# Kernel tuning notes

Measured on AMD Instinct MI355X. Metric: run time of the kernel, lower is better.

The kernel has to match this reference:

```python
import jax, jax.numpy as jnp
import numpy as np

N = 50000
E = 800000
P = 16
H = 128
NUM_LAYERS = 2


def _lin_params(key, fan_in, fan_out):
    k1, k2 = jax.random.split(key)
    bound = 1.0 / np.sqrt(fan_in)
    W = jax.random.uniform(k1, (fan_in, fan_out), jnp.float32, -bound, bound)
    b = jax.random.uniform(k2, (fan_out,), jnp.float32, -bound, bound)
    return W, b


def setup_inputs() -> dict:
    key = jax.random.key(0)
    ks = jax.random.split(key, 16)
    h = jax.random.normal(ks[0], (N, P), jnp.float32)
    x = jax.random.normal(ks[1], (N, 2), jnp.float32)
    edge_index = jax.random.randint(ks[2], (2, E), 0, N, jnp.int32)
    emb_W, emb_b = _lin_params(ks[3], P, H)
    e_W1, e_b1 = _lin_params(ks[4], 2 * H + 1, H)
    e_W2, e_b2 = _lin_params(ks[5], H, H)
    n_W1, n_b1 = _lin_params(ks[6], 2 * H, H)
    n_W2, n_b2 = _lin_params(ks[7], H, H)
    v_W1, v_b1 = _lin_params(ks[8], H, H)
    v_W2, v_b2 = _lin_params(ks[9], H, 2)
    c_W1, c_b1 = _lin_params(ks[10], H, H)
    c_W2, c_b2 = _lin_params(ks[11], H, 1)
    return dict(h=h, x=x, edge_index=edge_index,
                emb_W=emb_W, emb_b=emb_b,
                e_W1=e_W1, e_b1=e_b1, e_W2=e_W2, e_b2=e_b2,
                n_W1=n_W1, n_b1=n_b1, n_W2=n_W2, n_b2=n_b2,
                v_W1=v_W1, v_b1=v_b1, v_W2=v_W2, v_b2=v_b2,
                c_W1=c_W1, c_b1=c_b1, c_W2=c_W2, c_b2=c_b2)


def _mlp(z, W1, b1, W2, b2):
    return jnp.maximum(z @ W1 + b1, 0.0) @ W2 + b2


def reference(h, x, edge_index, emb_W, emb_b,
              e_W1, e_b1, e_W2, e_b2,
              n_W1, n_b1, n_W2, n_b2,
              v_W1, v_b1, v_W2, v_b2,
              c_W1, c_b1, c_W2, c_b2):
    row, col = edge_index[0], edge_index[1]
    n_nodes = h.shape[0]
    # edge count per source node for scatter-mean (0-count nodes stay 0)
    cnt = jax.ops.segment_sum(jnp.ones((row.shape[0],), h.dtype), row,
                              num_segments=n_nodes)
    denom = jnp.maximum(cnt, 1.0)[:, None]

    h = h @ emb_W + emb_b  # [N, H]
    v = None
    for _ in range(NUM_LAYERS):
        rel_pos = x[row] - x[col]                         # [E, 2]
        rel_dist = jnp.sum(rel_pos ** 2, axis=-1, keepdims=True)  # [E, 1]
        rel_theta = jnp.arctan2(rel_pos[:, 1], rel_pos[:, 0])     # [E]
        rel_pos2 = rel_dist * jnp.stack(
            [jnp.cos(2.0 * rel_theta), jnp.sin(2.0 * rel_theta)], axis=1)  # [E, 2]
        edge_feat = jnp.concatenate([h[row], h[col], rel_dist], axis=-1)   # [E, 2H+1]
        m_ij = _mlp(edge_feat, e_W1, e_b1, e_W2, e_b2)    # [E, H] (dropout = eval identity)
        m_i = jax.ops.segment_sum(m_ij, row, num_segments=n_nodes)  # [N, H]
        h = h + _mlp(jnp.concatenate([h, m_i], axis=-1), n_W1, n_b1, n_W2, n_b2)
        v = _mlp(h, v_W1, v_b1, v_W2, v_b2)               # [N, 2]
        coord = _mlp(m_ij, c_W1, c_b1, c_W2, c_b2)        # [E, 1]
        scat = jax.ops.segment_sum(rel_pos2 * coord, row, num_segments=n_nodes)
        v = v + scat / denom                              # scatter-mean
    # F.normalize(p=2, dim=-1, eps=1e-12)
    norm = jnp.linalg.norm(v, axis=-1, keepdims=True)
    v = v / jnp.maximum(norm, 1e-12)
    return h, x, v
```

## Files before the change

### kernel.cpp

```cpp
#include <hip/hip_runtime.h>
#include <hip/hip_fp16.h>

typedef _Float16 f16;
typedef unsigned short u16;
typedef f16 f16x2 __attribute__((ext_vector_type(2)));
typedef f16 f16x8 __attribute__((ext_vector_type(8)));
typedef float f32x4 __attribute__((ext_vector_type(4)));

constexpr int N_NODES = 50000;
constexpr int E_EDGES = 800000;
constexpr int NBINS   = 50176;
constexpr int NBLK    = 196;

constexpr size_t OFF_DEG   = 0;
constexpr size_t OFF_LOCEX = 200704;
constexpr size_t OFF_BSUM  = 401408;
constexpr size_t OFF_BOFF  = 402432;
constexpr size_t OFF_FILL  = 403456;
constexpr size_t OFF_SCAT  = 604160;
constexpr size_t OFF_SROW  = 1004160;
constexpr size_t OFF_SCOL  = 2604160;
constexpr size_t OFF_ZSUM  = 4204160;
constexpr size_t ZSH_BYTES = (size_t)N_NODES * 128 * 2;
constexpr size_t ZS_BYTES  = (size_t)N_NODES * 128 * 4;
constexpr size_t OFF_APRE  = OFF_ZSUM + ZS_BYTES;
constexpr size_t OFF_BPRE  = OFF_APRE + (size_t)N_NODES * 128 * 2;
constexpr size_t OFF_CMB   = OFF_BPRE + (size_t)N_NODES * 128 * 2;
constexpr size_t OFF_WX    = OFF_CMB + 65536;
constexpr size_t OFF_BVEC  = OFF_WX + 65536;
constexpr size_t OFF_BX    = OFF_BVEC + 512;
constexpr size_t OFF_WSWZ  = OFF_BX + 512;

__device__ __forceinline__ void split_f(float x, f16& h, f16& l) {
    h = (f16)x;
    l = (f16)(x - (float)h);
}

__device__ __forceinline__ f32x4 mfma3(f16x8 ah, f16x8 al, f16x8 bh, f16x8 bl, f32x4 acc) {
    acc = __builtin_amdgcn_mfma_f32_16x16x32_f16(ah, bh, acc, 0, 0, 0);
    acc = __builtin_amdgcn_mfma_f32_16x16x32_f16(al, bh, acc, 0, 0, 0);
    acc = __builtin_amdgcn_mfma_f32_16x16x32_f16(ah, bl, acc, 0, 0, 0);
    return acc;
}

__device__ __forceinline__ void pk_atomic_add(f16* addr, float a0, float a1) {
    __half2 hv = __floats2half2_rn(a0, a1);
    unsafeAtomicAdd((__half2*)addr, hv);
}

__global__ __launch_bounds__(256) void compose_kernel(
    const float* __restrict__ eW2, const float* __restrict__ eb2,
    const float* __restrict__ nW1, const float* __restrict__ cW1,
    const float* __restrict__ cb1,
    float* __restrict__ Wcmb, float* __restrict__ Wx,
    float* __restrict__ bvec, float* __restrict__ bx)
{
    const int gid = blockIdx.x * 256 + threadIdx.x;
    if (gid < 16384) {
        const int k = gid >> 7, j = gid & 127;
        float s = 0.f;
        for (int t2 = 0; t2 < 128; ++t2) s += eW2[k * 128 + t2] * nW1[(128 + t2) * 128 + j];
        Wcmb[gid] = s;
    } else if (gid < 32768) {
        const int e = gid - 16384;
        const int k = e >> 7, j = e & 127;
        float s = 0.f;
        for (int t2 = 0; t2 < 128; ++t2) s += eW2[k * 128 + t2] * cW1[t2 * 128 + j];
        Wx[e] = s;
    } else if (gid < 32896) {
        const int j = gid - 32768;
        float s = 0.f;
        for (int k = 0; k < 128; ++k) s += eb2[k] * nW1[(128 + k) * 128 + j];
        bvec[j] = s;
    } else if (gid < 33024) {
        const int j = gid - 32896;
        float s = cb1[j];
        for (int k = 0; k < 128; ++k) s += eb2[k] * cW1[k * 128 + j];
        bx[j] = s;
    }
}

__global__ __launch_bounds__(256) void prep_kernel(
    const float* __restrict__ eW1, const float* __restrict__ nW1,
    const float* __restrict__ nW2, const float* __restrict__ vW1,
    const float* __restrict__ Wcmb, const float* __restrict__ Wx,
    f16* __restrict__ Wpres, f16* __restrict__ nW1cs,
    f16* __restrict__ nW2s, f16* __restrict__ vW1s, f16* __restrict__ Wxs)
{
    const int gid = blockIdx.x * 256 + threadIdx.x;
    int K32, e, which; f16* out;
    if (gid < 32768)       { which = 0; out = Wpres; K32 = 4; e = gid; }
    else if (gid < 65536)  { which = 1; out = nW1cs; K32 = 8; e = gid - 32768; }
    else if (gid < 81920)  { which = 2; out = nW2s;  K32 = 4; e = gid - 65536; }
    else if (gid < 98304)  { which = 3; out = vW1s;  K32 = 4; e = gid - 81920; }
    else                   { which = 4; out = Wxs;   K32 = 4; e = gid - 98304; }
    const int per = 512 * K32;
    const int ct = e / per, rem = e % per;
    const int kk = rem >> 9, lane = (rem >> 3) & 63, j = rem & 7;
    const int col = ct * 16 + (lane & 15);
    const int k = kk * 32 + ((lane >> 4) & 3) * 8 + j;
    float v;
    if (which == 0)      v = (col < 128) ? eW1[k * 128 + col] : eW1[(128 + k) * 128 + (col - 128)];
    else if (which == 1) v = (k < 128) ? nW1[k * 128 + col] : Wcmb[(k - 128) * 128 + col];
    else if (which == 2) v = nW2[k * 128 + col];
    else if (which == 3) v = vW1[k * 128 + col];
    else                 v = Wx[k * 128 + col];
    f16 h, l; split_f(v, h, l);
    const int base = ((ct * K32 + kk) * 2) * 512 + lane * 8 + j;
    out[base] = h;
    out[base + 512] = l;
}

__global__ __launch_bounds__(256) void hist_kernel(const int* __restrict__ eidx,
                                                   int* __restrict__ deg) {
    const int e = blockIdx.x * 256 + threadIdx.x;
    if (e < E_EDGES) atomicAdd(&deg[eidx[e]], 1);
}

__global__ __launch_bounds__(256) void scan1_kernel(const int* __restrict__ deg,
                                                    int* __restrict__ locEx,
                                                    int* __restrict__ blockSum) {
    __shared__ int s[256];
    const int t = threadIdx.x;
    const int gid = blockIdx.x * 256 + t;
    const int v = deg[gid];
    s[t] = v;
    __syncthreads();
    for (int off = 1; off < 256; off <<= 1) {
        const int add = (t >= off) ? s[t - off] : 0;
        __syncthreads();
        s[t] += add;
        __syncthreads();
    }
    locEx[gid] = s[t] - v;
    if (t == 255) blockSum[blockIdx.x] = s[255];
}

__global__ __launch_bounds__(256) void scan2_kernel(const int* __restrict__ blockSum,
                                                    int* __restrict__ blockOff) {
    __shared__ int s[256];
    const int t = threadIdx.x;
    const int v = (t < NBLK) ? blockSum[t] : 0;
    s[t] = v;
    __syncthreads();
    for (int off = 1; off < 256; off <<= 1) {
        const int add = (t >= off) ? s[t - off] : 0;
        __syncthreads();
        s[t] += add;
        __syncthreads();
    }
    if (t < NBLK) blockOff[t] = s[t] - v;
}

__global__ __launch_bounds__(256) void scatter_kernel(const int* __restrict__ eidx,
        const int* __restrict__ locEx, const int* __restrict__ blockOff,
        int* __restrict__ fill, u16* __restrict__ srow, u16* __restrict__ scol) {
    const int e = blockIdx.x * 256 + threadIdx.x;
    if (e >= E_EDGES) return;
    const int r = eidx[e], c = eidx[E_EDGES + e];
    const int pos = blockOff[r >> 8] + locEx[r] + atomicAdd(&fill[r], 1);
    srow[pos] = (u16)r;
    scol[pos] = (u16)c;
}

__global__ __launch_bounds__(256) void embed_kernel(
    const float* __restrict__ h_in, const float* __restrict__ embW,
    const float* __restrict__ embb, float* __restrict__ h)
{
    const int gid = blockIdx.x * 256 + threadIdx.x;
    if (gid >= N_NODES * 128) return;
    const int n = gid >> 7, j = gid & 127;
    float s = embb[j];
#pragma unroll
    for (int p = 0; p < 16; ++p) s += h_in[n * 16 + p] * embW[p * 128 + j];
    h[gid] = s;
}

__device__ __forceinline__ void stage8(const float* src, f16* dst) {
    const float4 f0 = *(const float4*)src;
    const float4 f1 = *(const float4*)(src + 4);
    const float xs[8] = {f0.x, f0.y, f0.z, f0.w, f1.x, f1.y, f1.z, f1.w};
    f16x8 vh, vl;
#pragma unroll
    for (int i = 0; i < 8; ++i) { f16 hh, ll; split_f(xs[i], hh, ll); vh[i] = hh; vl[i] = ll; }
    *(f16x8*)dst = vh;
    *(f16x8*)(dst + 8) = vl;
}

__global__ __launch_bounds__(256, 4) void pre_kernel(
    const float* __restrict__ h, const f16* __restrict__ Wpres,
    const float* __restrict__ eb1,
    f16* __restrict__ Apre, f16* __restrict__ Bpre)
{
    constexpr int S = 264;
    __shared__ f16 smA[64 * S];
    const int t = threadIdx.x;
    const int base = blockIdx.x * 64;
    const int lane = t & 63, w = t >> 6, qq = lane >> 4, nn = lane & 15;

#pragma unroll
    for (int it = 0; it < 4; ++it) {
        const int idx = it * 256 + t;
        const int el = idx >> 4, seg = idx & 15;
        const int node = base + el;
        f16* dst = &smA[el * S + seg * 16];
        if (node < N_NODES) {
            stage8(h + (size_t)node * 128 + seg * 8, dst);
        } else {
            *(f16x8*)dst = (f16x8)(f16)0.f;
            *(f16x8*)(dst + 8) = (f16x8)(f16)0.f;
        }
    }
    __syncthreads();

#pragma unroll
    for (int half = 0; half < 2; ++half) {
        f32x4 acc[4][2] = {};
        for (int kk = 0; kk < 4; ++kk) {
            f16x8 Ah[4], Al[4];
#pragma unroll
            for (int rt = 0; rt < 4; ++rt) {
                const f16* ap = &smA[(rt * 16 + nn) * S + (kk * 4 + qq) * 16];
                Ah[rt] = *(const f16x8*)ap;
                Al[rt] = *(const f16x8*)(ap + 8);
            }
#pragma unroll
            for (int c = 0; c < 2; ++c) {
                const int ct = w * 4 + half * 2 + c;
                const f16* bp = Wpres + (size_t)((ct * 4 + kk) * 2) * 512 + lane * 8;
                const f16x8 Bh = *(const f16x8*)bp;
                const f16x8 Bl = *(const f16x8*)(bp + 512);
#pragma unroll
                for (int rt = 0; rt < 4; ++rt)
                    acc[rt][c] = mfma3(Ah[rt], Al[rt], Bh, Bl, acc[rt][c]);
            }
        }
#pragma unroll
        for (int c = 0; c < 2; ++c) {
            const int col = w * 64 + half * 32 + c * 16 + nn;
#pragma unroll
            for (int rt = 0; rt < 4; ++rt) {
#pragma unroll
                for (int r = 0; r < 4; ++r) {
                    const int el = rt * 16 + qq * 4 + r;
                    const int node = base + el;
                    if (node < N_NODES) {
                        const float v = acc[rt][c][r];
                        if (col < 128) Apre[(size_t)node * 128 + col] = (f16)(v + eb1[col]);
                        else           Bpre[(size_t)node * 128 + (col - 128)] = (f16)v;
                    }
                }
            }
        }
    }
}

__global__ __launch_bounds__(256, 8) void edge_z_kernel(
    const u16* __restrict__ srow, const u16* __restrict__ scol,
    const float* __restrict__ x,
    const f16* __restrict__ Apre, const f16* __restrict__ Bpre,
    const float* __restrict__ wlast,
    f16* __restrict__ zsumh)
{
    constexpr int S2 = 136;
    __shared__ f16 smZ[64 * S2];
    __shared__ int smRow[64], smCol[64];
    __shared__ float smRd[64];
    const int t = threadIdx.x;
    const int base = blockIdx.x * 64;
    if (t < 64) {
        const int e = base + t;
        const int r = (int)srow[e], c = (int)scol[e];
        smRow[t] = r; smCol[t] = c;
        const float dx = x[2 * r] - x[2 * c];
        const float dy = x[2 * r + 1] - x[2 * c + 1];
        smRd[t] = dx * dx + dy * dy;
    }
    __syncthreads();

    const int seg = t & 15;
    const float4 w0 = *(const float4*)(wlast + seg * 8);
    const float4 w1 = *(const float4*)(wlast + seg * 8 + 4);
    const float wl[8] = {w0.x, w0.y, w0.z, w0.w, w1.x, w1.y, w1.z, w1.w};
#pragma unroll
    for (int it = 0; it < 4; ++it) {
        const int el = it * 16 + (t >> 4);
        const int rn = smRow[el], cn = smCol[el];
        const f16x8 av = *(const f16x8*)(Apre + (size_t)rn * 128 + seg * 8);
        const f16x8 bv = *(const f16x8*)(Bpre + (size_t)cn * 128 + seg * 8);
        const float rd = smRd[el];
        f16x8 vz;
#pragma unroll
        for (int i = 0; i < 8; ++i)
            vz[i] = (f16)fmaxf((float)av[i] + (float)bv[i] + rd * wl[i], 0.f);
        *(f16x8*)&smZ[el * S2 + seg * 8] = vz;
    }
    __syncthreads();

    const int p = t & 63, g = t >> 6;
    float a0 = 0.f, a1 = 0.f;
    int prev = smRow[g * 16];
#pragma unroll
    for (int e = g * 16; e < g * 16 + 16; ++e) {
        const int rw = smRow[e];
        if (rw != prev) {
            pk_atomic_add(&zsumh[(size_t)prev * 128 + 2 * p], a0, a1);
            a0 = a1 = 0.f; prev = rw;
        }
        const f16x2 v = *(const f16x2*)&smZ[e * S2 + 2 * p];
        a0 += (float)v[0]; a1 += (float)v[1];
    }
    pk_atomic_add(&zsumh[(size_t)prev * 128 + 2 * p], a0, a1);
}

__global__ __launch_bounds__(256, 8) void edge_coord_kernel(
    const u16* __restrict__ srow, const u16* __restrict__ scol,
    const float* __restrict__ x,
    const f16* __restrict__ Apre, const f16* __restrict__ Bpre,
    const float* __restrict__ wlast,
    const f16* __restrict__ Wxs, const float* __restrict__ bx,
    const float* __restrict__ cW2, const float* __restrict__ cb2,
    f16* __restrict__ zsumh, float* __restrict__ scat)
{
    constexpr int S2 = 136;
    __shared__ f16 smZ[64 * S2];
    __shared__ int smRow[64], smCol[64];
    __shared__ float smRd[64], smP2x[64], smP2y[64];
    __shared__ float smPart[4][64];

    const int t = threadIdx.x;
    const int base = blockIdx.x * 64;
    const int lane = t & 63, w = t >> 6, qq = lane >> 4, nn = lane & 15;

    if (t < 64) {
        const int e = base + t;
        const int r = (int)srow[e], c = (int)scol[e];
        smRow[t] = r; smCol[t] = c;
        const float dx = x[2 * r] - x[2 * c];
        const float dy = x[2 * r + 1] - x[2 * c + 1];
        smRd[t] = dx * dx + dy * dy;
        smP2x[t] = dx * dx - dy * dy;
        smP2y[t] = 2.0f * dx * dy;
    }
    __syncthreads();

    {
        const int seg = t & 15;
        const float4 w0 = *(const float4*)(wlast + seg * 8);
        const float4 w1 = *(const float4*)(wlast + seg * 8 + 4);
        const float wl[8] = {w0.x, w0.y, w0.z, w0.w, w1.x, w1.y, w1.z, w1.w};
#pragma unroll
        for (int it = 0; it < 4; ++it) {
            const int el = it * 16 + (t >> 4);
            const int rn = smRow[el], cn = smCol[el];
            const f16x8 av = *(const f16x8*)(Apre + (size_t)rn * 128 + seg * 8);
            const f16x8 bv = *(const f16x8*)(Bpre + (size_t)cn * 128 + seg * 8);
            const float rd = smRd[el];
            f16x8 vz;
#pragma unroll
            for (int i = 0; i < 8; ++i)
                vz[i] = (f16)fmaxf((float)av[i] + (float)bv[i] + rd * wl[i], 0.f);
            *(f16x8*)&smZ[el * S2 + seg * 8] = vz;
        }
    }
    __syncthreads();

    {
        const int p = t & 63, g = t >> 6;
        float a0 = 0.f, a1 = 0.f;
        int prev = smRow[g * 16];
#pragma unroll
        for (int e = g * 16; e < g * 16 + 16; ++e) {
            const int rw = smRow[e];
            if (rw != prev) {
                pk_atomic_add(&zsumh[(size_t)prev * 128 + 2 * p], a0, a1);
                a0 = a1 = 0.f; prev = rw;
            }
            const f16x2 v = *(const f16x2*)&smZ[e * S2 + 2 * p];
            a0 += (float)v[0]; a1 += (float)v[1];
        }
        pk_atomic_add(&zsumh[(size_t)prev * 128 + 2 * p], a0, a1);
    }

    f32x4 acc3[4][2] = {};
    for (int kk = 0; kk < 4; ++kk) {
        f16x8 A[4];
#pragma unroll
        for (int rt = 0; rt < 4; ++rt)
            A[rt] = *(const f16x8*)&smZ[(rt * 16 + nn) * S2 + (kk * 4 + qq) * 8];
#pragma unroll
        for (int c = 0; c < 2; ++c) {
            const int ct = w * 2 + c;
            const f16x8 Bh = *(const f16x8*)(Wxs + (size_t)((ct * 4 + kk) * 2) * 512 + lane * 8);
#pragma unroll
            for (int rt = 0; rt < 4; ++rt)
                acc3[rt][c] = __builtin_amdgcn_mfma_f32_16x16x32_f16(A[rt], Bh, acc3[rt][c], 0, 0, 0);
        }
    }
    float p3[4][4];
#pragma unroll
    for (int rt = 0; rt < 4; ++rt)
#pragma unroll
        for (int r = 0; r < 4; ++r) p3[rt][r] = 0.f;
#pragma unroll
    for (int c = 0; c < 2; ++c) {
        const int col = w * 32 + c * 16 + nn;
        const float c1 = bx[col];
        const float w2 = cW2[col];
#pragma unroll
        for (int rt = 0; rt < 4; ++rt)
#pragma unroll
            for (int r = 0; r < 4; ++r)
                p3[rt][r] += fmaxf(acc3[rt][c][r] + c1, 0.f) * w2;
    }
#pragma unroll
    for (int off = 1; off < 16; off <<= 1)
#pragma unroll
        for (int rt = 0; rt < 4; ++rt)
#pragma unroll
            for (int r = 0; r < 4; ++r) p3[rt][r] += __shfl_xor(p3[rt][r], off);
    if (nn == 0) {
#pragma unroll
        for (int rt = 0; rt < 4; ++rt)
#pragma unroll
            for (int r = 0; r < 4; ++r)
                smPart[w][rt * 16 + qq * 4 + r] = p3[rt][r];
    }
    __syncthreads();
    if (t < 64) {
        const float co = smPart[0][t] + smPart[1][t] + smPart[2][t] + smPart[3][t] + cb2[0];
        const int rw = smRow[t];
        atomicAdd(&scat[2 * rw],     smP2x[t] * co);
        atomicAdd(&scat[2 * rw + 1], smP2y[t] * co);
    }
}

__global__ __launch_bounds__(256, 4) void node_kernel(
    float* __restrict__ h, f16* __restrict__ zsumh,
    const int* __restrict__ deg,
    const f16* __restrict__ nW1cs, const float* __restrict__ nb1,
    const float* __restrict__ bvec,
    const f16* __restrict__ nW2s, const float* __restrict__ nb2)
{
    constexpr int S = 264;
    __shared__ f16 smA[64 * S];
    __shared__ float smDeg[64];
    const int t = threadIdx.x;
    const int base = blockIdx.x * 64;
    const int lane = t & 63, w = t >> 6, qq = lane >> 4, nn = lane & 15;

    if (t < 64) smDeg[t] = (float)deg[base + t];

    f32x4 acc1[4][2] = {};
    for (int chunk = 0; chunk < 2; ++chunk) {
        if (chunk) __syncthreads();
#pragma unroll
        for (int it = 0; it < 4; ++it) {
            const int idx = it * 256 + t;
            const int el = idx >> 4, seg = idx & 15;
            const int node = base + el;
            f16* dst = &smA[el * S + seg * 16];
            if (node < N_NODES) {
                if (chunk == 0) {
                    stage8(h + (size_t)node * 128 + seg * 8, dst);
                } else {
                    f16* src = zsumh + (size_t)node * 128 + seg * 8;
                    const f16x8 v = *(const f16x8*)src;
                    *(f16x8*)dst = v;
                    *(f16x8*)(dst + 8) = (f16x8)(f16)0.f;
                    *(f16x8*)src = (f16x8)(f16)0.f;
                }
            } else {
                *(f16x8*)dst = (f16x8)(f16)0.f;
                *(f16x8*)(dst + 8) = (f16x8)(f16)0.f;
            }
        }
        __syncthreads();
        for (int kk = 0; kk < 4; ++kk) {
            f16x8 Ah[4], Al[4];
#pragma unroll
            for (int rt = 0; rt < 4; ++rt) {
                const f16* ap = &smA[(rt * 16 + nn) * S + (kk * 4 + qq) * 16];
                Ah[rt] = *(const f16x8*)ap;
                Al[rt] = *(const f16x8*)(ap + 8);
            }
            const int kkg = chunk * 4 + kk;
#pragma unroll
            for (int c = 0; c < 2; ++c) {
                const int ct = w * 2 + c;
                const f16* bp = nW1cs + (size_t)((ct * 8 + kkg) * 2) * 512 + lane * 8;
                const f16x8 Bh = *(const f16x8*)bp;
                const f16x8 Bl = *(const f16x8*)(bp + 512);
#pragma unroll
                for (int rt = 0; rt < 4; ++rt)
                    acc1[rt][c] = mfma3(Ah[rt], Al[rt], Bh, Bl, acc1[rt][c]);
            }
        }
    }
    __syncthreads();
#pragma unroll
    for (int c = 0; c < 2; ++c) {
        const int col = w * 32 + c * 16 + nn;
        const float b1 = nb1[col];
        const float bv = bvec[col];
#pragma unroll
        for (int rt = 0; rt < 4; ++rt) {
#pragma unroll
            for (int r = 0; r < 4; ++r) {
                const int el = rt * 16 + qq * 4 + r;
                const float z = fmaxf(acc1[rt][c][r] + b1 + smDeg[el] * bv, 0.f);
                f16 zh, zl; split_f(z, zh, zl);
                f16* zp = &smA[el * S + (col >> 3) * 16 + (col & 7)];
                zp[0] = zh; zp[8] = zl;
            }
        }
    }
    __syncthreads();

    f32x4 acc2[4][2] = {};
    for (int kk = 0; kk < 4; ++kk) {
        f16x8 Ah[4], Al[4];
#pragma unroll
        for (int rt = 0; rt < 4; ++rt) {
            const f16* ap = &smA[(rt * 16 + nn) * S + (kk * 4 + qq) * 16];
            Ah[rt] = *(const f16x8*)ap;
            Al[rt] = *(const f16x8*)(ap + 8);
        }
#pragma unroll
        for (int c = 0; c < 2; ++c) {
            const int ct = w * 2 + c;
            const f16* bp = nW2s + (size_t)((ct * 4 + kk) * 2) * 512 + lane * 8;
            const f16x8 Bh = *(const f16x8*)bp;
            const f16x8 Bl = *(const f16x8*)(bp + 512);
#pragma unroll
            for (int rt = 0; rt < 4; ++rt)
                acc2[rt][c] = mfma3(Ah[rt], Al[rt], Bh, Bl, acc2[rt][c]);
        }
    }
#pragma unroll
    for (int c = 0; c < 2; ++c) {
        const int col = w * 32 + c * 16 + nn;
        const float b2 = nb2[col];
#pragma unroll
        for (int rt = 0; rt < 4; ++rt) {
#pragma unroll
            for (int r = 0; r < 4; ++r) {
                const int el = rt * 16 + qq * 4 + r;
                const int node = base + el;
                if (node < N_NODES) {
                    const size_t ix = (size_t)node * 128 + col;
                    h[ix] = h[ix] + acc2[rt][c][r] + b2;
                }
            }
        }
    }
}

__global__ __launch_bounds__(256, 4) void final_kernel(
    const float* __restrict__ h, const float* __restrict__ x,
    const f16* __restrict__ vW1s, const float* __restrict__ vb1,
    const float* __restrict__ vW2, const float* __restrict__ vb2,
    const float* __restrict__ scat, const int* __restrict__ deg,
    float* __restrict__ out)
{
    constexpr int S = 264;
    __shared__ f16 smA[64 * S];
    const int t = threadIdx.x;
    const int base = blockIdx.x * 64;
    const int lane = t & 63, w = t >> 6, qq = lane >> 4, nn = lane & 15;

#pragma unroll
    for (int it = 0; it < 4; ++it) {
        const int idx = it * 256 + t;
        const int el = idx >> 4, seg = idx & 15;
        const int node = base + el;
        f16* dst = &smA[el * S + seg * 16];
        if (node < N_NODES) {
            stage8(h + (size_t)node * 128 + seg * 8, dst);
        } else {
            *(f16x8*)dst = (f16x8)(f16)0.f;
            *(f16x8*)(dst + 8) = (f16x8)(f16)0.f;
        }
    }
    __syncthreads();

    f32x4 acc1[4][2] = {};
    for (int kk = 0; kk < 4; ++kk) {
        f16x8 Ah[4], Al[4];
#pragma unroll
        for (int rt = 0; rt < 4; ++rt) {
            const f16* ap = &smA[(rt * 16 + nn) * S + (kk * 4 + qq) * 16];
            Ah[rt] = *(const f16x8*)ap;
            Al[rt] = *(const f16x8*)(ap + 8);
        }
#pragma unroll
        for (int c = 0; c < 2; ++c) {
            const int ct = w * 2 + c;
            const f16* bp = vW1s + (size_t)((ct * 4 + kk) * 2) * 512 + lane * 8;
            const f16x8 Bh = *(const f16x8*)bp;
            const f16x8 Bl = *(const f16x8*)(bp + 512);
#pragma unroll
            for (int rt = 0; rt < 4; ++rt)
                acc1[rt][c] = mfma3(Ah[rt], Al[rt], Bh, Bl, acc1[rt][c]);
        }
    }
    __syncthreads();
#pragma unroll
    for (int c = 0; c < 2; ++c) {
        const int col = w * 32 + c * 16 + nn;
        const float b1 = vb1[col];
#pragma unroll
        for (int rt = 0; rt < 4; ++rt) {
#pragma unroll
            for (int r = 0; r < 4; ++r) {
                const int el = rt * 16 + qq * 4 + r;
                const float z = fmaxf(acc1[rt][c][r] + b1, 0.f);
                f16 zh, zl; split_f(z, zh, zl);
                f16* zp = &smA[el * S + (col >> 3) * 16 + (col & 7)];
                zp[0] = zh; zp[8] = zl;
            }
        }
    }
    __syncthreads();

    float* out_x = out + (size_t)N_NODES * 128;
    float* out_v = out_x + (size_t)N_NODES * 2;
    if (t < 128) {
        const int node = base + (t >> 1);
        if (node < N_NODES) out_x[node * 2 + (t & 1)] = x[node * 2 + (t & 1)];
    }
    if (t < 128) {
        const int rl = t >> 1, comp = t & 1;
        const int node = base + rl;
        float s = 0.f;
        if (node < N_NODES) {
            s = vb2[comp];
            for (int k = 0; k < 128; ++k) {
                const f16* zp = &smA[rl * S + (k >> 3) * 16 + (k & 7)];
                const float z = (float)zp[0] + (float)zp[8];
                s += z * vW2[k * 2 + comp];
            }
            const float dn = fmaxf((float)deg[node], 1.0f);
            s += scat[node * 2 + comp] / dn;
        }
        const float other = __shfl_xor(s, 1);
        if (node < N_NODES) {
            const float nrm = sqrtf(s * s + other * other);
            out_v[node * 2 + comp] = s / fmaxf(nrm, 1e-12f);
        }
    }
}

extern "C" void kernel_launch(void* const* d_in, const int* in_sizes, int n_in,
                              void* d_out, int out_size, void* d_ws, size_t ws_size,
                              hipStream_t stream) {
    const float* h_in = (const float*)d_in[0];
    const float* x    = (const float*)d_in[1];
    const int*   eidx = (const int*)d_in[2];
    const float* embW = (const float*)d_in[3];
    const float* embb = (const float*)d_in[4];
    const float* eW1  = (const float*)d_in[5];
    const float* eb1  = (const float*)d_in[6];
    const float* eW2  = (const float*)d_in[7];
    const float* eb2  = (const float*)d_in[8];
    const float* nW1  = (const float*)d_in[9];
    const float* nb1  = (const float*)d_in[10];
    const float* nW2  = (const float*)d_in[11];
    const float* nb2  = (const float*)d_in[12];
    const float* vW1  = (const float*)d_in[13];
    const float* vb1  = (const float*)d_in[14];
    const float* vW2  = (const float*)d_in[15];
    const float* vb2  = (const float*)d_in[16];
    const float* cW1  = (const float*)d_in[17];
    const float* cb1  = (const float*)d_in[18];
    const float* cW2  = (const float*)d_in[19];
    const float* cb2  = (const float*)d_in[20];

    char* ws = (char*)d_ws;
    int* deg    = (int*)(ws + OFF_DEG);
    int* locEx  = (int*)(ws + OFF_LOCEX);
    int* bsum   = (int*)(ws + OFF_BSUM);
    int* boff   = (int*)(ws + OFF_BOFF);
    int* fill   = (int*)(ws + OFF_FILL);
    float* scat = (float*)(ws + OFF_SCAT);
    u16* srow   = (u16*)(ws + OFF_SROW);
    u16* scol   = (u16*)(ws + OFF_SCOL);
    f16* zsumh  = (f16*)(ws + OFF_ZSUM);
    f16* Apre   = (f16*)(ws + OFF_APRE);
    f16* Bpre   = (f16*)(ws + OFF_BPRE);
    float* Wcmb = (float*)(ws + OFF_CMB);
    float* Wx   = (float*)(ws + OFF_WX);
    float* bvec = (float*)(ws + OFF_BVEC);
    float* bx   = (float*)(ws + OFF_BX);
    f16* Wpres  = (f16*)(ws + OFF_WSWZ);
    f16* nW1cs  = Wpres + 65536;
    f16* nW2s   = nW1cs + 65536;
    f16* vW1s   = nW2s + 32768;
    f16* Wxs    = vW1s + 32768;

    float* hcur = (float*)d_out;

    hipMemsetAsync(ws, 0, OFF_SROW, stream);
    hipMemsetAsync(zsumh, 0, ZSH_BYTES, stream);

    compose_kernel<<<129, 256, 0, stream>>>(eW2, eb2, nW1, cW1, cb1, Wcmb, Wx, bvec, bx);
    prep_kernel<<<448, 256, 0, stream>>>(eW1, nW1, nW2, vW1, Wcmb, Wx,
                                         Wpres, nW1cs, nW2s, vW1s, Wxs);
    hist_kernel<<<(E_EDGES + 255) / 256, 256, 0, stream>>>(eidx, deg);
    scan1_kernel<<<NBLK, 256, 0, stream>>>(deg, locEx, bsum);
    scan2_kernel<<<1, 256, 0, stream>>>(bsum, boff);
    scatter_kernel<<<(E_EDGES + 255) / 256, 256, 0, stream>>>(eidx, locEx, boff,
                                                              fill, srow, scol);
    embed_kernel<<<(N_NODES * 128 + 255) / 256, 256, 0, stream>>>(h_in, embW, embb, hcur);

    const float* wlast = eW1 + 256 * 128;

    pre_kernel<<<(N_NODES + 63) / 64, 256, 0, stream>>>(hcur, Wpres, eb1, Apre, Bpre);
    edge_z_kernel<<<E_EDGES / 64, 256, 0, stream>>>(srow, scol, x, Apre, Bpre, wlast, zsumh);
    node_kernel<<<(N_NODES + 63) / 64, 256, 0, stream>>>(hcur, zsumh, deg,
        nW1cs, nb1, bvec, nW2s, nb2);

    pre_kernel<<<(N_NODES + 63) / 64, 256, 0, stream>>>(hcur, Wpres, eb1, Apre, Bpre);
    edge_coord_kernel<<<E_EDGES / 64, 256, 0, stream>>>(srow, scol, x, Apre, Bpre, wlast,
        Wxs, bx, cW2, cb2, zsumh, scat);
    node_kernel<<<(N_NODES + 63) / 64, 256, 0, stream>>>(hcur, zsumh, deg,
        nW1cs, nb1, bvec, nW2s, nb2);

    final_kernel<<<(N_NODES + 63) / 64, 256, 0, stream>>>(hcur, x,
        vW1s, vb1, vW2, vb2, scat, deg, (float*)d_out);
}
```

Baseline: 584.6 us.

## Fuse node update with next pre-projection and final MLP; XCD-swizzle edge blocks

The node update kernel is merged with the following pre-projection in layer one and with the final velocity MLP in layer two. The updated h is kept in shared memory as split fp16 hi/lo pairs and reused directly, so h is not re-read from global memory and two launches are removed. Edge kernels also remap block indices so each XCD handles a contiguous range of edges, which should improve L2 locality on the sorted rows. The cost is higher register and shared-memory pressure in the fused kernels and extra barriers.

After: 653.5 us. +11.8%, slower.

```diff
diff --git a/kernel.cpp b/kernel.cpp
--- a/kernel.cpp
+++ b/kernel.cpp
@@ -46,6 +46,12 @@
 __device__ __forceinline__ void pk_atomic_add(f16* addr, float a0, float a1) {
     __half2 hv = __floats2half2_rn(a0, a1);
     unsafeAtomicAdd((__half2*)addr, hv);
+}
+
+__device__ __forceinline__ int xcd_swizzle(int wgid, int nwg) {
+    const int q = nwg >> 3, r = nwg & 7;
+    const int xcd = wgid & 7, i = wgid >> 3;
+    return (xcd < r ? xcd * (q + 1) : r * (q + 1) + (xcd - r) * q) + i;
 }
 
 __global__ __launch_bounds__(256) void compose_kernel(
@@ -267,7 +273,7 @@
     __shared__ int smRow[64], smCol[64];
     __shared__ float smRd[64];
     const int t = threadIdx.x;
-    const int base = blockIdx.x * 64;
+    const int base = xcd_swizzle(blockIdx.x, gridDim.x) * 64;
     if (t < 64) {
         const int e = base + t;
         const int r = (int)srow[e], c = (int)scol[e];
@@ -329,7 +335,7 @@
     __shared__ float smPart[4][64];
 
     const int t = threadIdx.x;
-    const int base = blockIdx.x * 64;
+    const int base = xcd_swizzle(blockIdx.x, gridDim.x) * 64;
     const int lane = t & 63, w = t >> 6, qq = lane >> 4, nn = lane & 15;
 
     if (t < 64) {
@@ -435,18 +441,15 @@
     }
 }
 
-__global__ __launch_bounds__(256, 4) void node_kernel(
+__device__ __forceinline__ void node_core(
     float* __restrict__ h, f16* __restrict__ zsumh,
     const int* __restrict__ deg,
     const f16* __restrict__ nW1cs, const float* __restrict__ nb1,
     const float* __restrict__ bvec,
-    const f16* __restrict__ nW2s, const float* __restrict__ nb2)
+    const f16* __restrict__ nW2s, const float* __restrict__ nb2,
+    f16* smA, float* smDeg, int t, int base)
 {
     constexpr int S = 264;
-    __shared__ f16 smA[64 * S];
-    __shared__ float smDeg[64];
-    const int t = threadIdx.x;
-    const int base = blockIdx.x * 64;
     const int lane = t & 63, w = t >> 6, qq = lane >> 4, nn = lane & 15;
 
     if (t < 64) smDeg[t] = (float)deg[base + t];
@@ -537,6 +540,7 @@
                 acc2[rt][c] = mfma3(Ah[rt], Al[rt], Bh, Bl, acc2[rt][c]);
         }
     }
+    __syncthreads();
 #pragma unroll
     for (int c = 0; c < 2; ++c) {
         const int col = w * 32 + c * 16 + nn;
@@ -549,40 +553,97 @@
                 const int node = base + el;
                 if (node < N_NODES) {
                     const size_t ix = (size_t)node * 128 + col;
-                    h[ix] = h[ix] + acc2[rt][c][r] + b2;
+                    const float hn = h[ix] + acc2[rt][c][r] + b2;
+                    h[ix] = hn;
+                    f16 hh, hl; split_f(hn, hh, hl);
+                    f16* hp = &smA[el * S + (col >> 3) * 16 + (col & 7)];
+                    hp[0] = hh; hp[8] = hl;
                 }
             }
         }
     }
-}
-
-__global__ __launch_bounds__(256, 4) void final_kernel(
-    const float* __restrict__ h, const float* __restrict__ x,
-    const f16* __restrict__ vW1s, const float* __restrict__ vb1,
-    const float* __restrict__ vW2, const float* __restrict__ vb2,
-    const float* __restrict__ scat, const int* __restrict__ deg,
-    float* __restrict__ out)
+    __syncthreads();
+}
+
+__global__ __launch_bounds__(256, 4) void node_pre_kernel(
+    float* __restrict__ h, f16* __restrict__ zsumh,
+    const int* __restrict__ deg,
+    const f16* __restrict__ nW1cs, const float* __restrict__ nb1,
+    const float* __restrict__ bvec,
+    const f16* __restrict__ nW2s, const float* __restrict__ nb2,
+    const f16* __restrict__ Wpres, const float* __restrict__ eb1,
+    f16* __restrict__ Apre, f16* __restrict__ Bpre)
 {
     constexpr int S = 264;
     __shared__ f16 smA[64 * S];
+    __shared__ float smDeg[64];
     const int t = threadIdx.x;
     const int base = blockIdx.x * 64;
     const int lane = t & 63, w = t >> 6, qq = lane >> 4, nn = lane & 15;
 
-#pragma unroll
-    for (int it = 0; it < 4; ++it) {
-        const int idx = it * 256 + t;
-        const int el = idx >> 4, seg = idx & 15;
-        const int node = base + el;
-        f16* dst = &smA[el * S + seg * 16];
-        if (node < N_NODES) {
-            stage8(h + (size_t)node * 128 + seg * 8, dst);
-        } else {
-            *(f16x8*)dst = (f16x8)(f16)0.f;
-            *(f16x8*)(dst + 8) = (f16x8)(f16)0.f;
-        }
-    }
-    __syncthreads();
+    node_core(h, zsumh, deg, nW1cs, nb1, bvec, nW2s, nb2, smA, smDeg, t, base);
+
+#pragma unroll
+    for (int half = 0; half < 2; ++half) {
+        f32x4 acc[4][2] = {};
+        for (int kk = 0; kk < 4; ++kk) {
+            f16x8 Ah[4], Al[4];
+#pragma unroll
+            for (int rt = 0; rt < 4; ++rt) {
+                const f16* ap = &smA[(rt * 16 + nn) * S + (kk * 4 + qq) * 16];
+                Ah[rt] = *(const f16x8*)ap;
+                Al[rt] = *(const f16x8*)(ap + 8);
+            }
+#pragma unroll
+            for (int c = 0; c < 2; ++c) {
+                const int ct = w * 4 + half * 2 + c;
+                const f16* bp = Wpres + (size_t)((ct * 4 + kk) * 2) * 512 + lane * 8;
+                const f16x8 Bh = *(const f16x8*)bp;
+                const f16x8 Bl = *(const f16x8*)(bp + 512);
+#pragma unroll
+                for (int rt = 0; rt < 4; ++rt)
+                    acc[rt][c] = mfma3(Ah[rt], Al[rt], Bh, Bl, acc[rt][c]);
+            }
+        }
+#pragma unroll
+        for (int c = 0; c < 2; ++c) {
+            const int col = w * 64 + half * 32 + c * 16 + nn;
+#pragma unroll
+            for (int rt = 0; rt < 4; ++rt) {
+#pragma unroll
+                for (int r = 0; r < 4; ++r) {
+                    const int el = rt * 16 + qq * 4 + r;
+                    const int node = base + el;
+                    if (node < N_NODES) {
+                        const float v = acc[rt][c][r];
+                        if (col < 128) Apre[(size_t)node * 128 + col] = (f16)(v + eb1[col]);
+                        else           Bpre[(size_t)node * 128 + (col - 128)] = (f16)v;
+                    }
+                }
+            }
+        }
+    }
+}
+
+__global__ __launch_bounds__(256, 4) void node_final_kernel(
+    float* __restrict__ h, f16* __restrict__ zsumh,
+    const int* __restrict__ deg,
+    const f16* __restrict__ nW1cs, const float* __restrict__ nb1,
+    const float* __restrict__ bvec,
+    const f16* __restrict__ nW2s, const float* __restrict__ nb2,
+    const f16* __restrict__ vW1s, const float* __restrict__ vb1,
+    const float* __restrict__ vW2, const float* __restrict__ vb2,
+    const float* __restrict__ scat, const float* __restrict__ x,
+    float* __restrict__ out)
+{
+    constexpr int S = 264;
+    __shared__ f16 smA[64 * S];
+    __shared__ float smDeg[64];
+    const int t = threadIdx.x;
+    const int base = blockIdx.x * 64;
+    const int lane = t & 63, w = t >> 6, qq = lane >> 4, nn = lane & 15;
+
+    node_core(h, zsumh, deg, nW1cs, nb1, bvec, nW2s, nb2, smA, smDeg, t, base);
 
     f32x4 acc1[4][2] = {};
     for (int kk = 0; kk < 4; ++kk) {
@@ -640,7 +701,7 @@
                 const float z = (float)zp[0] + (float)zp[8];
                 s += z * vW2[k * 2 + comp];
             }
-            const float dn = fmaxf((float)deg[node], 1.0f);
+            const float dn = fmaxf((float)smDeg[rl], 1.0f);
             s += scat[node * 2 + comp] / dn;
         }
         const float other = __shfl_xor(s, 1);
@@ -717,15 +778,11 @@
 
     pre_kernel<<<(N_NODES + 63) / 64, 256, 0, stream>>>(hcur, Wpres, eb1, Apre, Bpre);
     edge_z_kernel<<<E_EDGES / 64, 256, 0, stream>>>(srow, scol, x, Apre, Bpre, wlast, zsumh);
-    node_kernel<<<(N_NODES + 63) / 64, 256, 0, stream>>>(hcur, zsumh, deg,
-        nW1cs, nb1, bvec, nW2s, nb2);
-
-    pre_kernel<<<(N_NODES + 63) / 64, 256, 0, stream>>>(hcur, Wpres, eb1, Apre, Bpre);
+    node_pre_kernel<<<(N_NODES + 63) / 64, 256, 0, stream>>>(hcur, zsumh, deg,
+        nW1cs, nb1, bvec, nW2s, nb2, Wpres, eb1, Apre, Bpre);
+
     edge_coord_kernel<<<E_EDGES / 64, 256, 0, stream>>>(srow, scol, x, Apre, Bpre, wlast,
         Wxs, bx, cW2, cb2, zsumh, scat);
-    node_kernel<<<(N_NODES + 63) / 64, 256, 0, stream>>>(hcur, zsumh, deg,
-        nW1cs, nb1, bvec, nW2s, nb2);
-
-    final_kernel<<<(N_NODES + 63) / 64, 256, 0, stream>>>(hcur, x,
-        vW1s, vb1, vW2, vb2, scat, deg, (float*)d_out);
-}
+    node_final_kernel<<<(N_NODES + 63) / 64, 256, 0, stream>>>(hcur, zsumh, deg,
+        nW1cs, nb1, bvec, nW2s, nb2, vW1s, vb1, vW2, vb2, scat, x, (float*)d_out);
+}
```
